# Kernel optimization log

Hardware: AMD Instinct MI355X
Metric: run time of the kernel (lower is better)

## Reference

```python
import jax, jax.numpy as jnp
import numpy as np

# FNO 2D spectral conv: rfft2 -> keep 2 corner mode blocks -> complex einsum -> scatter -> irfft2
B, H, W, CIN, COUT = 8, 256, 256, 32, 32
M1, M2 = 16, 16
SCALE = 1.0 / (CIN * COUT)  # matches self.scale = 1/(in_channels*out_channels)


def setup_inputs() -> dict:
    key = jax.random.key(0)
    k1, k2, k3 = jax.random.split(key, 3)
    x = jax.random.normal(k1, (B, H, W, CIN), dtype=jnp.float32)  # channels_last input
    wshape = (2, CIN, COUT, M1, M2)  # (2**(ndims-1), in_c, out_c, m1, m2)
    w_real = (jax.random.uniform(k2, wshape, dtype=jnp.float32) * 2.0 - 1.0) * SCALE
    w_imag = (jax.random.uniform(k3, wshape, dtype=jnp.float32) * 2.0 - 1.0) * SCALE
    return {"x": x, "w_real": w_real, "w_imag": w_imag}


def reference(x, w_real, w_imag):
    w = jax.lax.complex(w_real, w_imag)  # complex64 spectral weights
    # channels_last -> channels_first: [B,H,W,C] -> [B,C,H,W]
    xc = jnp.transpose(x, (0, 3, 1, 2))
    x_ft = jnp.fft.rfft2(xc)  # [B, C, H, W//2+1] complex64
    # Two corner blocks along dim H (low and high freqs), low freqs along rfft dim.
    blocks = jnp.stack(
        [x_ft[:, :, :M1, :M2], x_ft[:, :, H - M1:, :M2]], axis=0
    )  # [2, B, Cin, M1, M2]
    # einsum 'wbi...,wio...->w...bo' (reordered here to wbohk; scatter layout equivalent)
    ob = jnp.einsum('wbihk,wiohk->wbohk', blocks, w)  # [2, B, Cout, M1, M2]
    out_ft = jnp.zeros((B, COUT, H, W // 2 + 1), dtype=ob.dtype)
    out_ft = out_ft.at[:, :, :M1, :M2].set(ob[0])
    out_ft = out_ft.at[:, :, H - M1:, :M2].set(ob[1])
    out = jnp.fft.irfft2(out_ft, s=(H, W))  # [B, Cout, H, W] float32
    # back to channels_last; activation is None (identity)
    return jnp.transpose(out, (0, 2, 3, 1))
```

## Files before the change

### kernel.cpp

```cpp
#include <hip/hip_runtime.h>
#include <math.h>


#define INV_HW (1.0f / 65536.0f)

__global__ void k_tw(float* __restrict__ E1, float* __restrict__ U,
                     float* __restrict__ E4) {
  int t = blockIdx.x * blockDim.x + threadIdx.x;
  const float step = 6.28318530717958647692f / 256.0f;
  if (t < 1024) {
    int w = t >> 3, kwp = t & 7;
    int me = (2 * kwp * w) & 255, mo = ((2 * kwp + 1) * w) & 255;
    float se, ce, so, co;
    sincosf(step * (float)me, &se, &ce);
    sincosf(step * (float)mo, &so, &co);
    ((float4*)E1)[t] = make_float4(ce, -se, co, -so);
  } else if (t < 1280) {
    int n = t - 1024;
    float s, c;
    sincosf(step * (float)n, &s, &c);
    ((float2*)U)[n] = make_float2(c, s);
  } else if (t < 2304) {
    int i = t - 1280;
    int w = i >> 3, q = i & 7;
    int me = (2 * q * w) & 255, mo = ((2 * q + 1) * w) & 255;
    float se, ce, so, co;
    sincosf(step * (float)me, &se, &ce);
    sincosf(step * (float)mo, &so, &co);
    float sc_e = (q == 0) ? INV_HW : 2.0f * INV_HW;
    float sc_o = 2.0f * INV_HW;
    ((float4*)E4)[i] = make_float4(sc_e * ce, sc_e * se, sc_o * co, sc_o * so);
  }
}

__global__ __launch_bounds__(256) void k_wdft(const float* __restrict__ x,
                                              const float* __restrict__ E1,
                                              float* __restrict__ T) {
  __shared__ __align__(16) float sx[32 * 260];
  __shared__ float4 sE[1024];
  int bh = blockIdx.x, t = threadIdx.x;
  const float4* e1g = (const float4*)E1;
#pragma unroll
  for (int i = 0; i < 4; ++i) sE[t + 256 * i] = e1g[t + 256 * i];
  const float4* src = (const float4*)(x + (size_t)bh * 8192);
#pragma unroll
  for (int i = 0; i < 8; ++i) {
    int j = t + 256 * i;
    float4 v = src[j];
    int w = j >> 3, c0 = (j & 7) * 4;
    sx[(c0 + 0) * 260 + w] = v.x;
    sx[(c0 + 1) * 260 + w] = v.y;
    sx[(c0 + 2) * 260 + w] = v.z;
    sx[(c0 + 3) * 260 + w] = v.w;
  }
  __syncthreads();
  int c = t >> 3, kwp = t & 7;
  const float* xr = sx + c * 260;
  const float4* eb = sE + kwp;
  float ar = 0, ai = 0, br = 0, bi = 0;
#pragma unroll 4
  for (int j = 0; j < 32; ++j) {
    float4 xa = *(const float4*)(xr + 4 * j);
    float4 xb = *(const float4*)(xr + 128 + 4 * j);
    float4 e0 = eb[(4 * j + 0) * 8];
    float4 e1 = eb[(4 * j + 1) * 8];
    float4 e2 = eb[(4 * j + 2) * 8];
    float4 e3 = eb[(4 * j + 3) * 8];
    float ye, yo;
    ye = xa.x + xb.x; yo = xa.x - xb.x;
    ar += ye * e0.x; ai += ye * e0.y; br += yo * e0.z; bi += yo * e0.w;
    ye = xa.y + xb.y; yo = xa.y - xb.y;
    ar += ye * e1.x; ai += ye * e1.y; br += yo * e1.z; bi += yo * e1.w;
    ye = xa.z + xb.z; yo = xa.z - xb.z;
    ar += ye * e2.x; ai += ye * e2.y; br += yo * e2.z; bi += yo * e2.w;
    ye = xa.w + xb.w; yo = xa.w - xb.w;
    ar += ye * e3.x; ai += ye * e3.y; br += yo * e3.z; bi += yo * e3.w;
  }
  ((float4*)(T + (size_t)bh * 1024))[t] = make_float4(ar, ai, br, bi);
}

__global__ __launch_bounds__(512) void k_hdft(const float* __restrict__ T,
                                              const float* __restrict__ U,
                                              float* __restrict__ X) {
  __shared__ __align__(16) float sT[8192];
  __shared__ float2 sU[256];
  __shared__ float4 sRed[256];
  int b = blockIdx.x >> 5, c = blockIdx.x & 31;
  int t = threadIdx.x;
  const float4* src = (const float4*)(T + (size_t)b * 262144 + c * 32);
  float4* dT = (float4*)sT;
#pragma unroll
  for (int i = 0; i < 4; ++i) {
    int j = t + 512 * i;
    dT[j] = src[(j >> 3) * 256 + (j & 7)];
  }
  if (t < 256) sU[t] = ((const float2*)U)[t];
  __syncthreads();
  int kw = t & 15, kh = (t >> 4) & 15, s = t >> 8;
  float sg = (kh & 1) ? -1.f : 1.f;
  int st1 = kh, st2 = (kh + 240) & 255;
  int ph1 = (st1 * (s * 64)) & 255;
  int ph2 = (st2 * (s * 64)) & 255;
  float x0r = 0, x0i = 0, x1r = 0, x1i = 0;
  int h0 = s * 64;
#pragma unroll 4
  for (int hh = 0; hh < 64; ++hh) {
    int h = h0 + hh;
    float2 t0 = *(const float2*)(sT + h * 32 + kw * 2);
    float2 t1 = *(const float2*)(sT + (h + 128) * 32 + kw * 2);
    float tpx = fmaf(sg, t1.x, t0.x);
    float tpy = fmaf(sg, t1.y, t0.y);
    float2 e1 = sU[ph1];
    float2 e2 = sU[ph2];
    x0r += tpx * e1.x + tpy * e1.y;
    x0i += tpy * e1.x - tpx * e1.y;
    x1r += tpx * e2.x + tpy * e2.y;
    x1i += tpy * e2.x - tpx * e2.y;
    ph1 = (ph1 + st1) & 255;
    ph2 = (ph2 + st2) & 255;
  }
  if (s == 1) sRed[t - 256] = make_float4(x0r, x0i, x1r, x1i);
  __syncthreads();
  if (s == 0) {
    float4 p = sRed[t];
    x0r += p.x; x0i += p.y; x1r += p.z; x1i += p.w;
    float2* Xb = (float2*)(X + (size_t)blockIdx.x * 1024);
    Xb[kh * 16 + kw] = make_float2(x0r, x0i);
    Xb[(kh + 16) * 16 + kw] = make_float2(x1r, x1i);
  }
}

__global__ __launch_bounds__(256) void k_mix(const float* __restrict__ X,
                                             const float* __restrict__ wr,
                                             const float* __restrict__ wi,
                                             float* __restrict__ Y) {
  __shared__ __align__(16) float sX[1024];
  int b = blockIdx.x >> 5, kh = blockIdx.x & 31;
  int blk = kh >> 4, khl = kh & 15;
  int t = threadIdx.x;
  {
    int i = t >> 3, p = t & 7;
    ((float4*)sX)[t] =
        *(const float4*)(X + (size_t)(b * 32 + i) * 1024 + kh * 32 + p * 4);
  }
  __syncthreads();
  int kw = t & 15, o = t >> 4;
  const float* wr0 = wr + (size_t)blk * 262144 + khl * 16 + kw;
  const float* wi0 = wi + (size_t)blk * 262144 + khl * 16 + kw;
  float y0r = 0, y0i = 0, y1r = 0, y1i = 0;
#pragma unroll 4
  for (int i = 0; i < 32; ++i) {
    float2 xv = *(const float2*)(sX + i * 32 + kw * 2);
    float a0 = wr0[i * 8192 + o * 256], b0 = wi0[i * 8192 + o * 256];
    float a1 = wr0[i * 8192 + (o + 16) * 256], b1 = wi0[i * 8192 + (o + 16) * 256];
    y0r += xv.x * a0 - xv.y * b0;
    y0i += xv.x * b0 + xv.y * a0;
    y1r += xv.x * a1 - xv.y * b1;
    y1i += xv.x * b1 + xv.y * a1;
  }
  float2* Yb = (float2*)(Y + (size_t)b * 32768);
  Yb[(o * 32 + kh) * 16 + kw] = make_float2(y0r, y0i);
  Yb[((o + 16) * 32 + kh) * 16 + kw] = make_float2(y1r, y1i);
}

__global__ __launch_bounds__(256) void k_hidft(const float* __restrict__ Y,
                                               const float* __restrict__ U,
                                               float* __restrict__ G) {
  __shared__ __align__(16) float4 sY4[256];
  __shared__ float2 sU[256];
  int bi = blockIdx.x;
  int b = bi >> 7, o = (bi >> 2) & 31, hc = bi & 3;
  int t = threadIdx.x;
  sY4[t] = ((const float4*)(Y + (size_t)(b * 32 + o) * 1024))[t];
  sU[t] = ((const float2*)U)[t];
  __syncthreads();
  int q = t & 7, hl = t >> 3;
  int h = hc * 32 + hl;
  float se0r = 0, se0i = 0, se1r = 0, se1i = 0;
  float so0r = 0, so0i = 0, so1r = 0, so1i = 0;
#pragma unroll 4
  for (int kh2 = 0; kh2 < 16; ++kh2) {
    int khe = 2 * kh2, kho = khe + 1;
    int khae = khe < 16 ? khe : khe + 224;
    int khao = kho < 16 ? kho : kho + 224;
    float2 ee = sU[(khae * h) & 255];
    float2 eo = sU[(khao * h) & 255];
    float4 yE = sY4[khe * 8 + q];
    float4 yO = sY4[kho * 8 + q];
    se0r += yE.x * ee.x - yE.y * ee.y;
    se0i += yE.x * ee.y + yE.y * ee.x;
    se1r += yE.z * ee.x - yE.w * ee.y;
    se1i += yE.z * ee.y + yE.w * ee.x;
    so0r += yO.x * eo.x - yO.y * eo.y;
    so0i += yO.x * eo.y + yO.y * eo.x;
    so1r += yO.z * eo.x - yO.w * eo.y;
    so1i += yO.z * eo.y + yO.w * eo.x;
  }
  float* g0 = G + (((size_t)b * 256 + h) * 32 + o) * 32 + 4 * q;
  float* g1 = G + (((size_t)b * 256 + h + 128) * 32 + o) * 32 + 4 * q;
  *(float4*)g0 = make_float4(se0r + so0r, se0i + so0i, se1r + so1r, se1i + so1i);
  *(float4*)g1 = make_float4(se0r - so0r, se0i - so0i, se1r - so1r, se1i - so1i);
}

__global__ __launch_bounds__(256) void k_widft(const float* __restrict__ G,
                                               const float* __restrict__ E4,
                                               float* __restrict__ out) {
  __shared__ float sG[32 * 33];
  __shared__ float4 sE4[1024];
  int bh = blockIdx.x, t = threadIdx.x;
  const float4* e4g = (const float4*)E4;
#pragma unroll
  for (int i = 0; i < 4; ++i) sE4[t + 256 * i] = e4g[t + 256 * i];
  {
    float4 v = ((const float4*)(G + (size_t)bh * 1024))[t];
    int o = t >> 3, p = t & 7;
    float* d = sG + o * 33 + p * 4;
    d[0] = v.x; d[1] = v.y; d[2] = v.z; d[3] = v.w;
  }
  __syncthreads();
  int o = t & 31, wb = t >> 5;
  float g[32];
#pragma unroll
  for (int k = 0; k < 32; ++k) g[k] = sG[o * 33 + k];
  float* ob = out + (size_t)bh * 8192 + o;
#pragma unroll 2
  for (int j = 0; j < 16; ++j) {
    int w = wb * 16 + j;
    float se = 0.f, so = 0.f;
#pragma unroll
    for (int q = 0; q < 8; ++q) {
      float4 e = sE4[w * 8 + q];
      se += g[4 * q] * e.x - g[4 * q + 1] * e.y;
      so += g[4 * q + 2] * e.z - g[4 * q + 3] * e.w;
    }
    ob[(size_t)w * 32] = se + so;
    ob[(size_t)(w + 128) * 32] = se - so;
  }
}

extern "C" void kernel_launch(void* const* d_in, const int* in_sizes, int n_in,
                              void* d_out, int out_size, void* d_ws, size_t ws_size,
                              hipStream_t stream) {
  const float* x = (const float*)d_in[0];
  const float* wr = (const float*)d_in[1];
  const float* wi = (const float*)d_in[2];
  float* out = (float*)d_out;
  float* ws = (float*)d_ws;

  float* E1 = ws;
  float* U  = ws + 4096;
  float* E4 = ws + 4608;
  float* T  = ws + 8704;
  float* X  = ws + 2105856;
  float* Y  = ws + 2368000;
  float* G  = T;

  k_tw<<<9, 256, 0, stream>>>(E1, U, E4);
  k_wdft<<<2048, 256, 0, stream>>>(x, E1, T);
  k_hdft<<<256, 512, 0, stream>>>(T, U, X);
  k_mix<<<256, 256, 0, stream>>>(X, wr, wi, Y);
  k_hidft<<<1024, 256, 0, stream>>>(Y, U, G);
  k_widft<<<2048, 256, 0, stream>>>(G, E4, out);
}
```

Measured before the change: 159.0 us.

## Restructure forward DFT stages with split-K partials and register-blocked W-DFT

The W-direction DFT becomes a two-level, Cooley-Tukey-style decomposition with 4x4 register blocking and a cross-wave shuffle reduction. This removes the transposed shared-memory staging and cuts twiddle traffic. The H-DFT is split over four H-quarters, writing partial spectra that the mix kernel sums, which gives 4x more blocks. The mix kernel splits its input-channel reduction across two block halves with float4 weight loads, and the H-IDFT sums those halves. The W-IDFT is rewritten so each thread keeps its twiddles in registers and writes float4 outputs. All this adds parallelism but also extra partial-sum buffers and extra global traffic.

```diff
diff --git a/kernel.cpp b/kernel.cpp
--- a/kernel.cpp
+++ b/kernel.cpp
@@ -4,24 +4,31 @@
 
 #define INV_HW (1.0f / 65536.0f)
 
-__global__ void k_tw(float* __restrict__ E1, float* __restrict__ U,
-                     float* __restrict__ E4) {
+__global__ void k_tw(float* __restrict__ Eo, float* __restrict__ Ei,
+                     float* __restrict__ U, float* __restrict__ E4) {
   int t = blockIdx.x * blockDim.x + threadIdx.x;
   const float step = 6.28318530717958647692f / 256.0f;
-  if (t < 1024) {
-    int w = t >> 3, kwp = t & 7;
-    int me = (2 * kwp * w) & 255, mo = ((2 * kwp + 1) * w) & 255;
-    float se, ce, so, co;
-    sincosf(step * (float)me, &se, &ce);
-    sincosf(step * (float)mo, &so, &co);
-    ((float4*)E1)[t] = make_float4(ce, -se, co, -so);
-  } else if (t < 1280) {
-    int n = t - 1024;
-    float s, c;
-    sincosf(step * (float)n, &s, &c);
+  if (t < 512) {
+    int j = t & 3, kwq = (t >> 2) & 3, w1 = (t >> 4) & 15, ws = t >> 8;
+    int kw = 4 * kwq + j, w = ws * 64 + 4 * w1;
+    int m = (kw * w) & 255;
+    float s, c; sincosf(step * (float)m, &s, &c);
+    int base = ((ws * 16 + w1) * 4 + kwq) * 8 + 2 * j;
+    Eo[base] = c; Eo[base + 1] = -s;
+  } else if (t < 576) {
+    int i = t - 512;
+    int j = i & 3, w0 = (i >> 2) & 3, kwq = i >> 4;
+    int kw = 4 * kwq + j;
+    int m = (kw * w0) & 255;
+    float s, c; sincosf(step * (float)m, &s, &c);
+    int base = (kwq * 4 + w0) * 8 + 2 * j;
+    Ei[base] = c; Ei[base + 1] = -s;
+  } else if (t < 832) {
+    int n = t - 576;
+    float s, c; sincosf(step * (float)n, &s, &c);
     ((float2*)U)[n] = make_float2(c, s);
-  } else if (t < 2304) {
-    int i = t - 1280;
+  } else if (t < 1856) {
+    int i = t - 832;
     int w = i >> 3, q = i & 7;
     int me = (2 * q * w) & 255, mo = ((2 * q + 1) * w) & 255;
     float se, ce, so, co;
@@ -34,136 +41,175 @@
 }
 
 __global__ __launch_bounds__(256) void k_wdft(const float* __restrict__ x,
-                                              const float* __restrict__ E1,
+                                              const float* __restrict__ Eo,
+                                              const float* __restrict__ Ei,
                                               float* __restrict__ T) {
-  __shared__ __align__(16) float sx[32 * 260];
-  __shared__ float4 sE[1024];
+  __shared__ __align__(16) float sx[8192];
+  __shared__ __align__(16) float sEo[1024];
+  __shared__ __align__(16) float sEi[128];
   int bh = blockIdx.x, t = threadIdx.x;
-  const float4* e1g = (const float4*)E1;
-#pragma unroll
-  for (int i = 0; i < 4; ++i) sE[t + 256 * i] = e1g[t + 256 * i];
   const float4* src = (const float4*)(x + (size_t)bh * 8192);
-#pragma unroll
-  for (int i = 0; i < 8; ++i) {
-    int j = t + 256 * i;
-    float4 v = src[j];
-    int w = j >> 3, c0 = (j & 7) * 4;
-    sx[(c0 + 0) * 260 + w] = v.x;
-    sx[(c0 + 1) * 260 + w] = v.y;
-    sx[(c0 + 2) * 260 + w] = v.z;
-    sx[(c0 + 3) * 260 + w] = v.w;
-  }
-  __syncthreads();
-  int c = t >> 3, kwp = t & 7;
-  const float* xr = sx + c * 260;
-  const float4* eb = sE + kwp;
-  float ar = 0, ai = 0, br = 0, bi = 0;
+  float4* dx = (float4*)sx;
+#pragma unroll
+  for (int i = 0; i < 8; ++i) dx[t + 256 * i] = src[t + 256 * i];
+  ((float4*)sEo)[t] = ((const float4*)Eo)[t];
+  if (t < 32) ((float4*)sEi)[t] = ((const float4*)Ei)[t];
+  __syncthreads();
+  int kwq = t >> 6, ws = (t >> 5) & 1, c = t & 31;
+  float ar[4][4], ai[4][4];
+#pragma unroll
+  for (int a = 0; a < 4; ++a)
+#pragma unroll
+    for (int b = 0; b < 4; ++b) { ar[a][b] = 0.f; ai[a][b] = 0.f; }
+  const float* xc = sx + c;
 #pragma unroll 4
-  for (int j = 0; j < 32; ++j) {
-    float4 xa = *(const float4*)(xr + 4 * j);
-    float4 xb = *(const float4*)(xr + 128 + 4 * j);
-    float4 e0 = eb[(4 * j + 0) * 8];
-    float4 e1 = eb[(4 * j + 1) * 8];
-    float4 e2 = eb[(4 * j + 2) * 8];
-    float4 e3 = eb[(4 * j + 3) * 8];
+  for (int w1 = 0; w1 < 16; ++w1) {
+    int wb = ws * 64 + 4 * w1;
+    float xa0 = xc[(wb + 0) * 32], xa1 = xc[(wb + 1) * 32];
+    float xa2 = xc[(wb + 2) * 32], xa3 = xc[(wb + 3) * 32];
+    float xb0 = xc[(wb + 128) * 32], xb1 = xc[(wb + 129) * 32];
+    float xb2 = xc[(wb + 130) * 32], xb3 = xc[(wb + 131) * 32];
+    const float4* ep = (const float4*)(sEo + ((ws * 16 + w1) * 4 + kwq) * 8);
+    float4 e01 = ep[0], e23 = ep[1];
     float ye, yo;
-    ye = xa.x + xb.x; yo = xa.x - xb.x;
-    ar += ye * e0.x; ai += ye * e0.y; br += yo * e0.z; bi += yo * e0.w;
-    ye = xa.y + xb.y; yo = xa.y - xb.y;
-    ar += ye * e1.x; ai += ye * e1.y; br += yo * e1.z; bi += yo * e1.w;
-    ye = xa.z + xb.z; yo = xa.z - xb.z;
-    ar += ye * e2.x; ai += ye * e2.y; br += yo * e2.z; bi += yo * e2.w;
-    ye = xa.w + xb.w; yo = xa.w - xb.w;
-    ar += ye * e3.x; ai += ye * e3.y; br += yo * e3.z; bi += yo * e3.w;
-  }
-  ((float4*)(T + (size_t)bh * 1024))[t] = make_float4(ar, ai, br, bi);
-}
-
-__global__ __launch_bounds__(512) void k_hdft(const float* __restrict__ T,
+    ye = xa0 + xb0; yo = xa0 - xb0;
+    ar[0][0] += ye * e01.x; ai[0][0] += ye * e01.y;
+    ar[0][1] += yo * e01.z; ai[0][1] += yo * e01.w;
+    ar[0][2] += ye * e23.x; ai[0][2] += ye * e23.y;
+    ar[0][3] += yo * e23.z; ai[0][3] += yo * e23.w;
+    ye = xa1 + xb1; yo = xa1 - xb1;
+    ar[1][0] += ye * e01.x; ai[1][0] += ye * e01.y;
+    ar[1][1] += yo * e01.z; ai[1][1] += yo * e01.w;
+    ar[1][2] += ye * e23.x; ai[1][2] += ye * e23.y;
+    ar[1][3] += yo * e23.z; ai[1][3] += yo * e23.w;
+    ye = xa2 + xb2; yo = xa2 - xb2;
+    ar[2][0] += ye * e01.x; ai[2][0] += ye * e01.y;
+    ar[2][1] += yo * e01.z; ai[2][1] += yo * e01.w;
+    ar[2][2] += ye * e23.x; ai[2][2] += ye * e23.y;
+    ar[2][3] += yo * e23.z; ai[2][3] += yo * e23.w;
+    ye = xa3 + xb3; yo = xa3 - xb3;
+    ar[3][0] += ye * e01.x; ai[3][0] += ye * e01.y;
+    ar[3][1] += yo * e01.z; ai[3][1] += yo * e01.w;
+    ar[3][2] += ye * e23.x; ai[3][2] += ye * e23.y;
+    ar[3][3] += yo * e23.z; ai[3][3] += yo * e23.w;
+  }
+  const float4* eip = (const float4*)(sEi + kwq * 32);
+  float Tr[4] = {0, 0, 0, 0}, Ti[4] = {0, 0, 0, 0};
+#pragma unroll
+  for (int w0 = 0; w0 < 4; ++w0) {
+    float4 g01 = eip[2 * w0], g23 = eip[2 * w0 + 1];
+    Tr[0] += ar[w0][0] * g01.x - ai[w0][0] * g01.y;
+    Ti[0] += ar[w0][0] * g01.y + ai[w0][0] * g01.x;
+    Tr[1] += ar[w0][1] * g01.z - ai[w0][1] * g01.w;
+    Ti[1] += ar[w0][1] * g01.w + ai[w0][1] * g01.z;
+    Tr[2] += ar[w0][2] * g23.x - ai[w0][2] * g23.y;
+    Ti[2] += ar[w0][2] * g23.y + ai[w0][2] * g23.x;
+    Tr[3] += ar[w0][3] * g23.z - ai[w0][3] * g23.w;
+    Ti[3] += ar[w0][3] * g23.w + ai[w0][3] * g23.z;
+  }
+#pragma unroll
+  for (int j = 0; j < 4; ++j) {
+    Tr[j] += __shfl_xor(Tr[j], 32);
+    Ti[j] += __shfl_xor(Ti[j], 32);
+  }
+  if (ws == 0) {
+    float* tp = T + (size_t)bh * 1024 + c * 32 + kwq * 8;
+    *(float4*)tp = make_float4(Tr[0], Ti[0], Tr[1], Ti[1]);
+    *(float4*)(tp + 4) = make_float4(Tr[2], Ti[2], Tr[3], Ti[3]);
+  }
+}
+
+__global__ __launch_bounds__(256) void k_hdft(const float* __restrict__ T,
                                               const float* __restrict__ U,
-                                              float* __restrict__ X) {
-  __shared__ __align__(16) float sT[8192];
+                                              float* __restrict__ Xp) {
+  __shared__ __align__(16) float sT[2048];
   __shared__ float2 sU[256];
-  __shared__ float4 sRed[256];
-  int b = blockIdx.x >> 5, c = blockIdx.x & 31;
+  int bi = blockIdx.x;
+  int b = bi >> 7, c = (bi >> 2) & 31, hq = bi & 3;
   int t = threadIdx.x;
-  const float4* src = (const float4*)(T + (size_t)b * 262144 + c * 32);
-  float4* dT = (float4*)sT;
-#pragma unroll
-  for (int i = 0; i < 4; ++i) {
-    int j = t + 512 * i;
-    dT[j] = src[(j >> 3) * 256 + (j & 7)];
-  }
-  if (t < 256) sU[t] = ((const float2*)U)[t];
-  __syncthreads();
-  int kw = t & 15, kh = (t >> 4) & 15, s = t >> 8;
-  float sg = (kh & 1) ? -1.f : 1.f;
-  int st1 = kh, st2 = (kh + 240) & 255;
-  int ph1 = (st1 * (s * 64)) & 255;
-  int ph2 = (st2 * (s * 64)) & 255;
+#pragma unroll
+  for (int it = 0; it < 2; ++it) {
+    int idx = t + 256 * it;
+    int row = idx >> 3, col = idx & 7;
+    int h = hq * 32 + (row & 31) + (row >> 5) * 128;
+    ((float4*)sT)[idx] =
+        *(const float4*)(T + (size_t)(b * 256 + h) * 1024 + c * 32 + col * 4);
+  }
+  sU[t] = ((const float2*)U)[t];
+  __syncthreads();
+  int khp = t >> 4, kw = t & 15;
+  int kha2 = khp + 240;
+  float sg = (khp & 1) ? -1.f : 1.f;
+  int f0 = hq * 32;
+  int ph1 = (khp * f0) & 255, ph2 = (kha2 * f0) & 255;
   float x0r = 0, x0i = 0, x1r = 0, x1i = 0;
-  int h0 = s * 64;
 #pragma unroll 4
-  for (int hh = 0; hh < 64; ++hh) {
-    int h = h0 + hh;
-    float2 t0 = *(const float2*)(sT + h * 32 + kw * 2);
-    float2 t1 = *(const float2*)(sT + (h + 128) * 32 + kw * 2);
+  for (int fl = 0; fl < 32; ++fl) {
+    float2 t0 = *(const float2*)(sT + fl * 32 + kw * 2);
+    float2 t1 = *(const float2*)(sT + (fl + 32) * 32 + kw * 2);
     float tpx = fmaf(sg, t1.x, t0.x);
     float tpy = fmaf(sg, t1.y, t0.y);
-    float2 e1 = sU[ph1];
-    float2 e2 = sU[ph2];
+    float2 e1 = sU[ph1], e2 = sU[ph2];
     x0r += tpx * e1.x + tpy * e1.y;
     x0i += tpy * e1.x - tpx * e1.y;
     x1r += tpx * e2.x + tpy * e2.y;
     x1i += tpy * e2.x - tpx * e2.y;
-    ph1 = (ph1 + st1) & 255;
-    ph2 = (ph2 + st2) & 255;
-  }
-  if (s == 1) sRed[t - 256] = make_float4(x0r, x0i, x1r, x1i);
-  __syncthreads();
-  if (s == 0) {
-    float4 p = sRed[t];
-    x0r += p.x; x0i += p.y; x1r += p.z; x1i += p.w;
-    float2* Xb = (float2*)(X + (size_t)blockIdx.x * 1024);
-    Xb[kh * 16 + kw] = make_float2(x0r, x0i);
-    Xb[(kh + 16) * 16 + kw] = make_float2(x1r, x1i);
-  }
-}
-
-__global__ __launch_bounds__(256) void k_mix(const float* __restrict__ X,
+    ph1 = (ph1 + khp) & 255;
+    ph2 = (ph2 + kha2) & 255;
+  }
+  float2* xb = (float2*)(Xp + (size_t)(hq * 256 + b * 32 + c) * 1024);
+  xb[khp * 16 + kw] = make_float2(x0r, x0i);
+  xb[(khp + 16) * 16 + kw] = make_float2(x1r, x1i);
+}
+
+__global__ __launch_bounds__(256) void k_mix(const float* __restrict__ Xp,
                                              const float* __restrict__ wr,
-                                             const float* __restrict__ wi,
-                                             float* __restrict__ Y) {
+                                             const float* __restrict__ wi_,
+                                             float* __restrict__ Yp) {
   __shared__ __align__(16) float sX[1024];
-  int b = blockIdx.x >> 5, kh = blockIdx.x & 31;
+  int bi = blockIdx.x;
+  int b = bi >> 6, kh = (bi >> 1) & 31, ih = bi & 1;
   int blk = kh >> 4, khl = kh & 15;
   int t = threadIdx.x;
   {
-    int i = t >> 3, p = t & 7;
-    ((float4*)sX)[t] =
-        *(const float4*)(X + (size_t)(b * 32 + i) * 1024 + kh * 32 + p * 4);
-  }
-  __syncthreads();
-  int kw = t & 15, o = t >> 4;
-  const float* wr0 = wr + (size_t)blk * 262144 + khl * 16 + kw;
-  const float* wi0 = wi + (size_t)blk * 262144 + khl * 16 + kw;
-  float y0r = 0, y0i = 0, y1r = 0, y1i = 0;
-#pragma unroll 4
-  for (int i = 0; i < 32; ++i) {
-    float2 xv = *(const float2*)(sX + i * 32 + kw * 2);
-    float a0 = wr0[i * 8192 + o * 256], b0 = wi0[i * 8192 + o * 256];
-    float a1 = wr0[i * 8192 + (o + 16) * 256], b1 = wi0[i * 8192 + (o + 16) * 256];
-    y0r += xv.x * a0 - xv.y * b0;
-    y0i += xv.x * b0 + xv.y * a0;
-    y1r += xv.x * a1 - xv.y * b1;
-    y1i += xv.x * b1 + xv.y * a1;
-  }
-  float2* Yb = (float2*)(Y + (size_t)b * 32768);
-  Yb[(o * 32 + kh) * 16 + kw] = make_float2(y0r, y0i);
-  Yb[((o + 16) * 32 + kh) * 16 + kw] = make_float2(y1r, y1i);
-}
-
-__global__ __launch_bounds__(256) void k_hidft(const float* __restrict__ Y,
+    float4 acc = make_float4(0.f, 0.f, 0.f, 0.f);
+#pragma unroll
+    for (int hq = 0; hq < 4; ++hq) {
+      float4 v = *(const float4*)(Xp + (size_t)(hq * 256 + b * 32 + (t >> 3)) * 1024 +
+                                  kh * 32 + (t & 7) * 4);
+      acc.x += v.x; acc.y += v.y; acc.z += v.z; acc.w += v.w;
+    }
+    ((float4*)sX)[t] = acc;
+  }
+  __syncthreads();
+  int o = t >> 3, kwq = (t >> 1) & 3, is = t & 1;
+  float yr[4] = {0, 0, 0, 0}, yi[4] = {0, 0, 0, 0};
+  size_t wbase = (size_t)blk * 262144 + (size_t)o * 256 + khl * 16 + kwq * 4;
+#pragma unroll
+  for (int ii = 0; ii < 8; ++ii) {
+    int i = ih * 16 + is * 8 + ii;
+    float4 a = *(const float4*)(wr + wbase + (size_t)i * 8192);
+    float4 bb = *(const float4*)(wi_ + wbase + (size_t)i * 8192);
+    float4 x01 = *(const float4*)(sX + i * 32 + kwq * 8);
+    float4 x23 = *(const float4*)(sX + i * 32 + kwq * 8 + 4);
+    yr[0] += x01.x * a.x - x01.y * bb.x; yi[0] += x01.x * bb.x + x01.y * a.x;
+    yr[1] += x01.z * a.y - x01.w * bb.y; yi[1] += x01.z * bb.y + x01.w * a.y;
+    yr[2] += x23.x * a.z - x23.y * bb.z; yi[2] += x23.x * bb.z + x23.y * a.z;
+    yr[3] += x23.z * a.w - x23.w * bb.w; yi[3] += x23.z * bb.w + x23.w * a.w;
+  }
+#pragma unroll
+  for (int j = 0; j < 4; ++j) {
+    yr[j] += __shfl_xor(yr[j], 1);
+    yi[j] += __shfl_xor(yi[j], 1);
+  }
+  if (is == 0) {
+    float* yp = Yp + (size_t)((ih * 8 + b) * 32 + o) * 1024 + kh * 32 + kwq * 8;
+    *(float4*)yp = make_float4(yr[0], yi[0], yr[1], yi[1]);
+    *(float4*)(yp + 4) = make_float4(yr[2], yi[2], yr[3], yi[3]);
+  }
+}
+
+__global__ __launch_bounds__(256) void k_hidft(const float* __restrict__ Yp,
                                                const float* __restrict__ U,
                                                float* __restrict__ G) {
   __shared__ __align__(16) float4 sY4[256];
@@ -171,7 +217,11 @@
   int bi = blockIdx.x;
   int b = bi >> 7, o = (bi >> 2) & 31, hc = bi & 3;
   int t = threadIdx.x;
-  sY4[t] = ((const float4*)(Y + (size_t)(b * 32 + o) * 1024))[t];
+  {
+    float4 va = ((const float4*)(Yp + (size_t)(b * 32 + o) * 1024))[t];
+    float4 vb = ((const float4*)(Yp + (size_t)(256 + b * 32 + o) * 1024))[t];
+    sY4[t] = make_float4(va.x + vb.x, va.y + vb.y, va.z + vb.z, va.w + vb.w);
+  }
   sU[t] = ((const float2*)U)[t];
   __syncthreads();
   int q = t & 7, hl = t >> 3;
@@ -205,36 +255,39 @@
 __global__ __launch_bounds__(256) void k_widft(const float* __restrict__ G,
                                                const float* __restrict__ E4,
                                                float* __restrict__ out) {
-  __shared__ float sG[32 * 33];
-  __shared__ float4 sE4[1024];
+  __shared__ __align__(16) float sG[1024];
+  __shared__ __align__(16) float4 sE4[1024];
   int bh = blockIdx.x, t = threadIdx.x;
+  ((float4*)sG)[t] = ((const float4*)(G + (size_t)bh * 1024))[t];
   const float4* e4g = (const float4*)E4;
 #pragma unroll
   for (int i = 0; i < 4; ++i) sE4[t + 256 * i] = e4g[t + 256 * i];
-  {
-    float4 v = ((const float4*)(G + (size_t)bh * 1024))[t];
-    int o = t >> 3, p = t & 7;
-    float* d = sG + o * 33 + p * 4;
-    d[0] = v.x; d[1] = v.y; d[2] = v.z; d[3] = v.w;
-  }
-  __syncthreads();
-  int o = t & 31, wb = t >> 5;
-  float g[32];
-#pragma unroll
-  for (int k = 0; k < 32; ++k) g[k] = sG[o * 33 + k];
-  float* ob = out + (size_t)bh * 8192 + o;
-#pragma unroll 2
-  for (int j = 0; j < 16; ++j) {
-    int w = wb * 16 + j;
-    float se = 0.f, so = 0.f;
-#pragma unroll
-    for (int q = 0; q < 8; ++q) {
-      float4 e = sE4[w * 8 + q];
-      se += g[4 * q] * e.x - g[4 * q + 1] * e.y;
-      so += g[4 * q + 2] * e.z - g[4 * q + 3] * e.w;
+  __syncthreads();
+  int og = t >> 7, w = t & 127;
+  float4 tw[8];
+#pragma unroll
+  for (int q = 0; q < 8; ++q) tw[q] = sE4[w * 8 + q];
+  float* ob = out + (size_t)bh * 8192 + w * 32 + og * 16;
+  float* ob2 = ob + 128 * 32;
+#pragma unroll
+  for (int g4 = 0; g4 < 4; ++g4) {
+    float s0[4], s1[4];
+#pragma unroll
+    for (int k = 0; k < 4; ++k) {
+      int o = og * 16 + g4 * 4 + k;
+      const float4* gp = (const float4*)(sG + o * 32);
+      float se = 0.f, so = 0.f;
+#pragma unroll
+      for (int q = 0; q < 8; ++q) {
+        float4 g = gp[q];
+        se += g.x * tw[q].x - g.y * tw[q].y;
+        so += g.z * tw[q].z - g.w * tw[q].w;
+      }
+      s0[k] = se + so;
+      s1[k] = se - so;
     }
-    ob[(size_t)w * 32] = se + so;
-    ob[(size_t)(w + 128) * 32] = se - so;
+    *(float4*)(ob + g4 * 4) = make_float4(s0[0], s0[1], s0[2], s0[3]);
+    *(float4*)(ob2 + g4 * 4) = make_float4(s1[0], s1[1], s1[2], s1[3]);
   }
 }
 
@@ -247,18 +300,19 @@
   float* out = (float*)d_out;
   float* ws = (float*)d_ws;
 
-  float* E1 = ws;
-  float* U  = ws + 4096;
-  float* E4 = ws + 4608;
-  float* T  = ws + 8704;
-  float* X  = ws + 2105856;
-  float* Y  = ws + 2368000;
+  float* Eo = ws;
+  float* Ei = ws + 1024;
+  float* U  = ws + 1280;
+  float* E4 = ws + 1792;
+  float* T  = ws + 6144;
+  float* Xp = ws + 2103296;
+  float* Yp = ws + 3151872;
   float* G  = T;
 
-  k_tw<<<9, 256, 0, stream>>>(E1, U, E4);
-  k_wdft<<<2048, 256, 0, stream>>>(x, E1, T);
-  k_hdft<<<256, 512, 0, stream>>>(T, U, X);
-  k_mix<<<256, 256, 0, stream>>>(X, wr, wi, Y);
-  k_hidft<<<1024, 256, 0, stream>>>(Y, U, G);
+  k_tw<<<8, 256, 0, stream>>>(Eo, Ei, U, E4);
+  k_wdft<<<2048, 256, 0, stream>>>(x, Eo, Ei, T);
+  k_hdft<<<1024, 256, 0, stream>>>(T, U, Xp);
+  k_mix<<<512, 256, 0, stream>>>(Xp, wr, wi, Yp);
+  k_hidft<<<1024, 256, 0, stream>>>(Yp, U, G);
   k_widft<<<2048, 256, 0, stream>>>(G, E4, out);
 }
```

Result: slower. 169.6 us (+6.7%).
